# Kernel optimization log

Hardware: AMD Instinct MI355X
Metric: run time of the kernel (lower is better)

The kernel has to match this reference:

```python
import jax, jax.numpy as jnp
import numpy as np

B, C, L, D, H = 8, 64, 256, 64, 4
HD = C // H  # head_dim = 16
EPS = 1e-5


def _conv(x, w):
    # x: [B,C,L,D], w: [O,I,kh,kw], stride 1, SAME padding (matches padding=1 for 3x3, 0 for 1x1)
    return jax.lax.conv_general_dilated(
        x, w, window_strides=(1, 1), padding='SAME',
        dimension_numbers=('NCHW', 'OIHW', 'NCHW'))


def setup_inputs() -> dict:
    rng = jax.random.key(0)
    ks = jax.random.split(rng, 10)
    n = lambda k, s: jax.random.normal(k, s, dtype=jnp.float32)
    xav3 = float(np.sqrt(6.0 / (C * 9 + C * 9)))  # xavier_uniform bound for 3x3 conv
    xav1 = float(np.sqrt(6.0 / (C + C)))
    u = lambda k, s, b: jax.random.uniform(k, s, jnp.float32, -b, b)
    return {
        'query': n(ks[0], (B, C, L, D)),
        'key': n(ks[1], (B, C, L, D)),
        'value': n(ks[2], (B, C, L, D)),
        'Wq': u(ks[3], (C, C, 3, 3), xav3),
        'Wk': u(ks[4], (C, C, 3, 3), xav3),
        'Wv': u(ks[5], (C, C, 3, 3), xav3),
        'Wo': u(ks[6], (C, C, 1, 1), xav1),
        'bo': jnp.zeros((C,), jnp.float32),
        'gamma': jnp.ones((C,), jnp.float32),
        'beta': jnp.zeros((C,), jnp.float32),
    }


def reference(query, key, value, Wq, Wk, Wv, Wo, bo, gamma, beta):
    identity = query
    # projections -> [B, H, HD, L, D]
    Q = _conv(query, Wq).reshape(B, H, HD, L, D)
    K = _conv(key, Wk).reshape(B, H, HD, L, D)
    V = _conv(value, Wv).reshape(B, H, HD, L, D)
    # attention over L, contraction over D; head_dim acts as an extra batch dim
    scores = jnp.einsum('bhcld,bhcmd->bhclm', Q, K) / jnp.sqrt(jnp.float32(HD))
    attn = jax.nn.softmax(scores, axis=-1)  # dropout is identity in eval mode
    out = jnp.einsum('bhclm,bhcmd->bhcld', attn, V).reshape(B, C, L, D)
    out = _conv(out, Wo) + bo[None, :, None, None] + identity
    # LayerNorm over channel dim (original permutes C last)
    mu = jnp.mean(out, axis=1, keepdims=True)
    var = jnp.var(out, axis=1, keepdims=True)
    out = (out - mu) * jax.lax.rsqrt(var + EPS)
    out = out * gamma[None, :, None, None] + beta[None, :, None, None]
    return out
```

## Files before the change

### kernel.cpp

```cpp
#include <hip/hip_runtime.h>

typedef _Float16 f16;
typedef f16   f16x8 __attribute__((ext_vector_type(8)));
typedef float f32x4 __attribute__((ext_vector_type(4)));

#define MFMA(a,b,c) __builtin_amdgcn_mfma_f32_16x16x32_f16(a,b,c,0,0,0)

__device__ __forceinline__ f32x4 fz4(){ f32x4 z; z[0]=0.f; z[1]=0.f; z[2]=0.f; z[3]=0.f; return z; }
__device__ __forceinline__ f16x8 hz8(){ f16x8 z;
#pragma unroll
  for(int i=0;i<8;++i) z[i]=(f16)0.f;
  return z; }

#define NBLK 256u

__device__ __forceinline__ void grid_barrier(unsigned* bar) {
  __syncthreads();
  if (threadIdx.x == 0) {
    __threadfence();
    unsigned gen  = atomicAdd(&bar[1], 0u);
    unsigned prev = atomicAdd(&bar[0], 1u);
    if (prev == NBLK - 1u) {
      atomicExch(&bar[0], 0u);
      __threadfence();
      atomicAdd(&bar[1], 1u);
    } else {
      while (atomicAdd(&bar[1], 0u) == gen) __builtin_amdgcn_s_sleep(2);
    }
    __threadfence();
  }
  __syncthreads();
}

__global__ __launch_bounds__(512, 2) void mega(
    const float* __restrict__ query, const float* __restrict__ key,
    const float* __restrict__ value,
    const float* __restrict__ Wq, const float* __restrict__ Wk,
    const float* __restrict__ Wv, const float* __restrict__ Wo,
    const float* __restrict__ bo, const float* __restrict__ gamma,
    const float* __restrict__ beta,
    f16* __restrict__ QKV, f16* __restrict__ AO,
    f16* WA, float* out, unsigned* bar)
{
  __shared__ f16 smem[32768];
  const int tid  = threadIdx.x;
  const int bid  = blockIdx.x;
  const int half = tid >> 8;
  const int ltid = tid & 255;
  const int lane = tid & 63;
  const int wvg  = tid >> 6;
  const int wvl  = (ltid >> 6);
  const int lr   = lane & 15, kh = lane >> 4;
  f16* hs = smem + half*16384;

  {
    int gid = bid*512 + tid;
    if (gid < 110592) {
      int t = gid / 36864, r = gid % 36864;
      const float* W = (t==0)?Wq:((t==1)?Wk:Wv);
      float sc = (t==0) ? 0.25f : 1.0f;
      int kstep = r >> 11, rem = r & 2047;
      int co = rem >> 5, rem2 = rem & 31;
      int kq = rem2 >> 3, j = rem2 & 7;
      int k = kstep*32 + kq*8 + j;
      int sp = k >> 6, ci = k & 63;
      int ky = sp/3, kx = sp - ky*3;
      WA[gid] = (f16)(W[((co*64+ci)*3+ky)*3+kx]*sc);
    }
  }
  grid_barrier(bar);

  for (int iter = 0; iter < 6; ++iter) {
    int w    = bid + (iter*2 + half)*256;
    int b    = w & 7;
    int rest = w >> 3;
    int t    = rest >> 7;
    int l0   = (rest & 127) * 2;
    const float* X = (t==0)?query:((t==1)?key:value);
    const f16* WAt = WA + t*36864;
    f16* Yt = QKV + (size_t)t*8388608;
    {
      int ci0 = (ltid & 31)*2;
      int row = (ltid >> 5) & 3;
      int dh  = (ltid >> 7) * 32;
      int gr  = l0 - 1 + row;
      bool valid = (unsigned)gr < 256u;
      int grc = valid ? gr : 0;
      const f32x4* s0 = (const f32x4*)(X + (((size_t)(b*64+ci0  )*256 + grc)*64 + dh));
      const f32x4* s1 = (const f32x4*)(X + (((size_t)(b*64+ci0+1)*256 + grc)*64 + dh));
#pragma unroll
      for (int q=0;q<8;++q) {
        f32x4 f0 = valid ? s0[q] : fz4();
        f32x4 f1 = valid ? s1[q] : fz4();
#pragma unroll
        for (int e=0;e<4;++e) {
          int d = dh + q*4 + e;
          int idx = ((row*64 + d)*64 + ci0) ^ ((d&7)<<3);
          unsigned int pk = (unsigned int)__builtin_bit_cast(unsigned short,(f16)f0[e])
                          | ((unsigned int)__builtin_bit_cast(unsigned short,(f16)f1[e]) << 16);
          *(unsigned int*)&hs[idx] = pk;
        }
      }
    }
    __syncthreads();
    f32x4 acc[4][2];
#pragma unroll
    for (int mt=0;mt<4;++mt){ acc[mt][0]=fz4(); acc[mt][1]=fz4(); }
    for (int kstep=0; kstep<18; ++kstep) {
      int sp = kstep >> 1;
      int sp3 = sp/3;
      int dl = sp3 - 1;
      int dd = (sp - sp3*3) - 1;
      int cib = (kstep & 1)*32;
      const f16* wp = WAt + kstep*2048 + lr*32 + kh*8;
      f16x8 a0 = *(const f16x8*)(wp);
      f16x8 a1 = *(const f16x8*)(wp + 512);
      f16x8 a2 = *(const f16x8*)(wp + 1024);
      f16x8 a3 = *(const f16x8*)(wp + 1536);
      f16x8 bb[2];
#pragma unroll
      for (int nt=0;nt<2;++nt) {
        int n = wvl*32 + nt*16 + lr;
        int lloc = n >> 6, d = n & 63;
        int dp = d + dd;
        bool v = (unsigned)dp < 64u;
        int dpc = dp & 63;
        int rowi = lloc + dl + 1;
        int idx = ((rowi*64 + dpc)*64 + cib + kh*8) ^ ((dpc&7)<<3);
        f16x8 tt = *(const f16x8*)&hs[idx];
        if (!v) tt = hz8();
        bb[nt] = tt;
      }
#pragma unroll
      for (int nt=0;nt<2;++nt) {
        acc[0][nt] = MFMA(a0, bb[nt], acc[0][nt]);
        acc[1][nt] = MFMA(a1, bb[nt], acc[1][nt]);
        acc[2][nt] = MFMA(a2, bb[nt], acc[2][nt]);
        acc[3][nt] = MFMA(a3, bb[nt], acc[3][nt]);
      }
    }
#pragma unroll
    for (int mt=0;mt<4;++mt)
#pragma unroll
    for (int nt=0;nt<2;++nt)
#pragma unroll
    for (int r=0;r<4;++r) {
      int co = mt*16 + kh*4 + r;
      int n = wvl*32 + nt*16 + lr;
      int lrow = l0 + (n>>6), d = n & 63;
      Yt[((size_t)(b*64+co)*256 + lrow)*64 + d] = (f16)acc[mt][nt][r];
    }
    __syncthreads();
  }
  grid_barrier(bar);

  for (int k2 = 0; k2 < 2; ++k2) {
    int idx = bid + k2*256;
    int bc = (idx & 7)*64 + (idx >> 3);
    const f16* Qs = QKV + (size_t)bc*16384;
    const f16* Ks = QKV +  8388608 + (size_t)bc*16384;
    const f16* Vs = QKV + 16777216 + (size_t)bc*16384;
    __syncthreads();
    {
      int m  = tid & 63;
      int dg = (tid >> 6) * 8;
#pragma unroll
      for (int pass=0; pass<4; ++pass) {
        int mm = m + pass*64;
        f16x8 v0 = *(const f16x8*)(Vs + mm*64 + dg);
#pragma unroll
        for (int e=0;e<8;++e){ int d=dg+e; smem[(d*256+mm) ^ ((d&7)<<3)] = v0[e]; }
      }
    }
    int l0g = wvg*32;
    f16x8 qf[2][2];
#pragma unroll
    for (int lt=0;lt<2;++lt)
#pragma unroll
    for (int ks=0;ks<2;++ks)
      qf[lt][ks] = *(const f16x8*)(Qs + (l0g + lt*16 + lr)*64 + ks*32 + kh*8);
    f32x4 O[2][4];
    float rm[2][4], rl[2][4];
#pragma unroll
    for (int lt=0;lt<2;++lt)
#pragma unroll
    for (int x=0;x<4;++x) { O[lt][x]=fz4(); rm[lt][x]=-1e30f; rl[lt][x]=0.f; }
    __syncthreads();
    f16* P = &smem[16384 + wvg*2048];
    for (int it=0; it<4; ++it) {
      int m0 = it*64;
      f32x4 s[2][4];
#pragma unroll
      for (int lt=0;lt<2;++lt)
#pragma unroll
      for (int mt=0;mt<4;++mt) s[lt][mt]=fz4();
#pragma unroll
      for (int ks=0;ks<2;++ks) {
        f16x8 kf[4];
#pragma unroll
        for (int mt=0;mt<4;++mt)
          kf[mt] = *(const f16x8*)(Ks + (m0 + mt*16 + lr)*64 + ks*32 + kh*8);
#pragma unroll
        for (int lt=0;lt<2;++lt)
#pragma unroll
        for (int mt=0;mt<4;++mt)
          s[lt][mt] = MFMA(qf[lt][ks], kf[mt], s[lt][mt]);
      }
#pragma unroll
      for (int lt=0;lt<2;++lt)
#pragma unroll
      for (int r=0;r<4;++r) {
        float tm = fmaxf(fmaxf(s[lt][0][r], s[lt][1][r]), fmaxf(s[lt][2][r], s[lt][3][r]));
#pragma unroll
        for (int off=1; off<16; off<<=1) tm = fmaxf(tm, __shfl_xor(tm, off));
        float mo = rm[lt][r];
        float mn = fmaxf(mo, tm);
        rm[lt][r] = mn;
        float corr = __expf(mo - mn);
        float sum = 0.f;
#pragma unroll
        for (int mt=0;mt<4;++mt) { float p = __expf(s[lt][mt][r] - mn); s[lt][mt][r] = p; sum += p; }
#pragma unroll
        for (int off=1; off<16; off<<=1) sum += __shfl_xor(sum, off);
        rl[lt][r] = rl[lt][r]*corr + sum;
#pragma unroll
        for (int dt=0;dt<4;++dt) O[lt][dt][r] *= corr;
      }
#pragma unroll
      for (int lt=0;lt<2;++lt)
#pragma unroll
      for (int mt=0;mt<4;++mt)
#pragma unroll
      for (int r=0;r<4;++r) {
        int row = lt*16 + kh*4 + r;
        P[(row*64 + mt*16 + lr) ^ ((row&7)<<3)] = (f16)s[lt][mt][r];
      }
#pragma unroll
      for (int ks=0;ks<2;++ks) {
        f16x8 pa[2], vb[4];
#pragma unroll
        for (int lt=0;lt<2;++lt) {
          int row = lt*16 + lr;
          pa[lt] = *(const f16x8*)&P[(row*64 + ks*32 + kh*8) ^ ((row&7)<<3)];
        }
#pragma unroll
        for (int dt=0;dt<4;++dt) {
          int d = dt*16 + lr;
          vb[dt] = *(const f16x8*)&smem[(d*256 + m0 + ks*32 + kh*8) ^ ((d&7)<<3)];
        }
#pragma unroll
        for (int lt=0;lt<2;++lt)
#pragma unroll
        for (int dt=0;dt<4;++dt)
          O[lt][dt] = MFMA(pa[lt], vb[dt], O[lt][dt]);
      }
    }
#pragma unroll
    for (int lt=0;lt<2;++lt)
#pragma unroll
    for (int r=0;r<4;++r) {
      float inv = 1.f / rl[lt][r];
      int row = l0g + lt*16 + kh*4 + r;
#pragma unroll
      for (int dt=0;dt<4;++dt)
        AO[(size_t)bc*16384 + row*64 + dt*16 + lr] = (f16)(O[lt][dt][r]*inv);
    }
  }
  grid_barrier(bar);

  for (int iter = 0; iter < 2; ++iter) {
    int w  = bid + (iter*2 + half)*256;
    int b  = w & 7;
    int p0 = (w >> 3) * 128;
    {
      int ci = ltid & 63;
      int pg = ltid >> 6;
      const f16* src = AO + (size_t)(b*64+ci)*16384 + p0 + pg*32;
      f16x8 v[4];
#pragma unroll
      for (int q=0;q<4;++q) v[q] = *(const f16x8*)(src + q*8);
#pragma unroll
      for (int q=0;q<4;++q)
#pragma unroll
      for (int e=0;e<8;++e) {
        int p = pg*32 + q*8 + e;
        hs[(p*64 + ci) ^ ((p&7)<<3)] = v[q][e];
      }
      int co  = ltid >> 2;
      int cig = (ltid & 3) * 16;
      const f32x4* wsrc = (const f32x4*)(Wo + co*64 + cig);
      f32x4 w0 = wsrc[0], w1 = wsrc[1], w2 = wsrc[2], w3 = wsrc[3];
      f16x8 g0, g1;
#pragma unroll
      for (int e=0;e<4;++e) { g0[e]=(f16)w0[e]; g0[4+e]=(f16)w1[e]; g1[e]=(f16)w2[e]; g1[4+e]=(f16)w3[e]; }
      *(f16x8*)&hs[8192 + ((co*64 + cig    ) ^ ((co&7)<<3))] = g0;
      *(f16x8*)&hs[8192 + ((co*64 + cig + 8) ^ ((co&7)<<3))] = g1;
    }
    __syncthreads();
    int n0 = wvl*32;
    f32x4 acc[4][2];
#pragma unroll
    for (int mt=0;mt<4;++mt){ acc[mt][0]=fz4(); acc[mt][1]=fz4(); }
#pragma unroll
    for (int ks=0;ks<2;++ks) {
      f16x8 a[4], bb[2];
#pragma unroll
      for (int mt=0;mt<4;++mt)
        a[mt] = *(const f16x8*)&hs[8192 + (((mt*16+lr)*64 + ks*32 + kh*8) ^ ((lr&7)<<3))];
#pragma unroll
      for (int nt=0;nt<2;++nt) {
        int p = n0 + nt*16 + lr;
        bb[nt] = *(const f16x8*)&hs[(p*64 + ks*32 + kh*8) ^ ((p&7)<<3)];
      }
#pragma unroll
      for (int mt=0;mt<4;++mt)
#pragma unroll
      for (int nt=0;nt<2;++nt)
        acc[mt][nt] = MFMA(a[mt], bb[nt], acc[mt][nt]);
    }
    float vals[4][2][4];
    float sum0=0.f, sq0=0.f, sum1=0.f, sq1=0.f;
#pragma unroll
    for (int mt=0;mt<4;++mt)
#pragma unroll
    for (int nt=0;nt<2;++nt)
#pragma unroll
    for (int r=0;r<4;++r) {
      int co = mt*16 + kh*4 + r;
      int p  = p0 + n0 + nt*16 + lr;
      float v = acc[mt][nt][r] + bo[co] + query[(size_t)(b*64+co)*16384 + p];
      vals[mt][nt][r] = v;
      if (nt==0) { sum0 += v; sq0 += v*v; } else { sum1 += v; sq1 += v*v; }
    }
#pragma unroll
    for (int off=16; off<64; off<<=1) {
      sum0 += __shfl_xor(sum0, off); sq0 += __shfl_xor(sq0, off);
      sum1 += __shfl_xor(sum1, off); sq1 += __shfl_xor(sq1, off);
    }
    float mu0 = sum0*(1.f/64.f), var0 = sq0*(1.f/64.f) - mu0*mu0, rs0 = rsqrtf(var0 + 1e-5f);
    float mu1 = sum1*(1.f/64.f), var1 = sq1*(1.f/64.f) - mu1*mu1, rs1 = rsqrtf(var1 + 1e-5f);
#pragma unroll
    for (int mt=0;mt<4;++mt)
#pragma unroll
    for (int nt=0;nt<2;++nt)
#pragma unroll
    for (int r=0;r<4;++r) {
      int co = mt*16 + kh*4 + r;
      int p  = p0 + n0 + nt*16 + lr;
      float mu = nt ? mu1 : mu0;
      float rs = nt ? rs1 : rs0;
      out[(size_t)(b*64+co)*16384 + p] = (vals[mt][nt][r] - mu)*rs*gamma[co] + beta[co];
    }
    __syncthreads();
  }
}

extern "C" void kernel_launch(void* const* d_in, const int* in_sizes, int n_in,
                              void* d_out, int out_size, void* d_ws, size_t ws_size,
                              hipStream_t stream)
{
  const float* query = (const float*)d_in[0];
  const float* key   = (const float*)d_in[1];
  const float* value = (const float*)d_in[2];
  const float* Wq = (const float*)d_in[3];
  const float* Wk = (const float*)d_in[4];
  const float* Wv = (const float*)d_in[5];
  const float* Wo = (const float*)d_in[6];
  const float* bo = (const float*)d_in[7];
  const float* gamma = (const float*)d_in[8];
  const float* beta  = (const float*)d_in[9];
  char* ws = (char*)d_ws;
  f16*      QKV  = (f16*)ws;
  f16*      AO   = (f16*)(ws + (size_t)50331648);
  f16*      WA   = (f16*)d_out;
  float*    outp = (float*)d_out;
  unsigned* bar  = (unsigned*)((char*)d_out + (size_t)(1<<20));

  hipMemsetAsync(bar, 0, 64, stream);
  mega<<<dim3(NBLK), dim3(512), 0, stream>>>(
      query, key, value, Wq, Wk, Wv, Wo, bo, gamma, beta,
      QKV, AO, WA, outp, bar);
}
```

Before: 238.8 us.

## Replace global grid barrier with per-batch group barriers of 32 blocks

Every phase of the kernel turns out to touch only data for batch bid&7. The single 256-block grid barrier is therefore replaced by eight independent 32-block group barriers, and each group builds its own copy of the converted weights inside its batch's slice of the output buffer. This cuts atomic contention on the barrier and lets batches move through phases without waiting on stragglers in other batches. In exchange, the weight conversion runs eight times over, and the host issues eight small memsets instead of one.

```diff
diff --git a/kernel.cpp b/kernel.cpp
--- a/kernel.cpp
+++ b/kernel.cpp
@@ -14,18 +14,19 @@
 
 #define NBLK 256u
 
-__device__ __forceinline__ void grid_barrier(unsigned* bar) {
+__device__ __forceinline__ void group_barrier(unsigned* gbar) {
   __syncthreads();
   if (threadIdx.x == 0) {
     __threadfence();
-    unsigned gen  = atomicAdd(&bar[1], 0u);
-    unsigned prev = atomicAdd(&bar[0], 1u);
-    if (prev == NBLK - 1u) {
-      atomicExch(&bar[0], 0u);
+    unsigned gen0 = __hip_atomic_load(&gbar[32], __ATOMIC_RELAXED, __HIP_MEMORY_SCOPE_AGENT);
+    unsigned p = atomicAdd(&gbar[0], 1u);
+    if (p == 31u) {
+      atomicExch(&gbar[0], 0u);
       __threadfence();
-      atomicAdd(&bar[1], 1u);
+      atomicAdd(&gbar[32], 1u);
     } else {
-      while (atomicAdd(&bar[1], 0u) == gen) __builtin_amdgcn_s_sleep(2);
+      while (__hip_atomic_load(&gbar[32], __ATOMIC_RELAXED, __HIP_MEMORY_SCOPE_AGENT) == gen0)
+        __builtin_amdgcn_s_sleep(2);
     }
     __threadfence();
   }
@@ -40,7 +41,7 @@
     const float* __restrict__ bo, const float* __restrict__ gamma,
     const float* __restrict__ beta,
     f16* __restrict__ QKV, f16* __restrict__ AO,
-    f16* WA, float* out, unsigned* bar)
+    char* outbase, unsigned* )
 {
   __shared__ f16 smem[32768];
   const int tid  = threadIdx.x;
@@ -53,22 +54,24 @@
   const int lr   = lane & 15, kh = lane >> 4;
   f16* hs = smem + half*16384;
 
-  {
-    int gid = bid*512 + tid;
-    if (gid < 110592) {
-      int t = gid / 36864, r = gid % 36864;
-      const float* W = (t==0)?Wq:((t==1)?Wk:Wv);
-      float sc = (t==0) ? 0.25f : 1.0f;
-      int kstep = r >> 11, rem = r & 2047;
-      int co = rem >> 5, rem2 = rem & 31;
-      int kq = rem2 >> 3, j = rem2 & 7;
-      int k = kstep*32 + kq*8 + j;
-      int sp = k >> 6, ci = k & 63;
-      int ky = sp/3, kx = sp - ky*3;
-      WA[gid] = (f16)(W[((co*64+ci)*3+ky)*3+kx]*sc);
-    }
-  }
-  grid_barrier(bar);
+  const int g = bid & 7;
+  f16*      WAg  = (f16*)(outbase + (size_t)g*(4u<<20));
+  unsigned* gbar = (unsigned*)(outbase + (size_t)g*(4u<<20) + (2u<<20));
+  float*    out  = (float*)outbase;
+
+  for (int e = (bid >> 3)*512 + tid; e < 110592; e += 16384) {
+    int t = e / 36864, r = e % 36864;
+    const float* W = (t==0)?Wq:((t==1)?Wk:Wv);
+    float sc = (t==0) ? 0.25f : 1.0f;
+    int kstep = r >> 11, rem = r & 2047;
+    int co = rem >> 5, rem2 = rem & 31;
+    int kq = rem2 >> 3, j = rem2 & 7;
+    int k = kstep*32 + kq*8 + j;
+    int sp = k >> 6, ci = k & 63;
+    int ky = sp/3, kx = sp - ky*3;
+    WAg[e] = (f16)(W[((co*64+ci)*3+ky)*3+kx]*sc);
+  }
+  group_barrier(gbar);
 
   for (int iter = 0; iter < 6; ++iter) {
     int w    = bid + (iter*2 + half)*256;
@@ -77,7 +80,7 @@
     int t    = rest >> 7;
     int l0   = (rest & 127) * 2;
     const float* X = (t==0)?query:((t==1)?key:value);
-    const f16* WAt = WA + t*36864;
+    const f16* WAt = WAg + t*36864;
     f16* Yt = QKV + (size_t)t*8388608;
     {
       int ci0 = (ltid & 31)*2;
@@ -152,7 +155,7 @@
     }
     __syncthreads();
   }
-  grid_barrier(bar);
+  group_barrier(gbar);
 
   for (int k2 = 0; k2 < 2; ++k2) {
     int idx = bid + k2*256;
@@ -266,7 +269,7 @@
         AO[(size_t)bc*16384 + row*64 + dt*16 + lr] = (f16)(O[lt][dt][r]*inv);
     }
   }
-  grid_barrier(bar);
+  group_barrier(gbar);
 
   for (int iter = 0; iter < 2; ++iter) {
     int w  = bid + (iter*2 + half)*256;
@@ -372,12 +375,11 @@
   char* ws = (char*)d_ws;
   f16*      QKV  = (f16*)ws;
   f16*      AO   = (f16*)(ws + (size_t)50331648);
-  f16*      WA   = (f16*)d_out;
-  float*    outp = (float*)d_out;
-  unsigned* bar  = (unsigned*)((char*)d_out + (size_t)(1<<20));
-
-  hipMemsetAsync(bar, 0, 64, stream);
+  char*     outb = (char*)d_out;
+
+  for (int g = 0; g < 8; ++g)
+    hipMemsetAsync(outb + (size_t)g*(4u<<20) + (2u<<20), 0, 256, stream);
   mega<<<dim3(NBLK), dim3(512), 0, stream>>>(
       query, key, value, Wq, Wk, Wv, Wo, bo, gamma, beta,
-      QKV, AO, WA, outp, bar);
+      QKV, AO, outb, (unsigned*)nullptr);
 }
```

Result: faster. 212.3 us (-11.1%).
